# Performance work log

Hardware: AMD Instinct MI355X
Metric: run time of the kernel (lower is better)

## Reference

```python
import jax, jax.numpy as jnp
import numpy as np

N_NODES = 100000
N_EDGES = 3200000
IN_DIM = 128
H1, F1 = 8, 8          # layer1: 8 heads x 8 feats -> concat 64
N_CLASSES = 40         # layer2: 1 head -> classes
NEG_SLOPE = 0.2        # GAT LeakyReLU slope


def setup_inputs() -> dict:
    key = jax.random.key(0)
    ks = jax.random.split(key, 8)
    x = jax.random.normal(ks[0], (N_NODES, IN_DIM), dtype=jnp.float32)
    adj = jax.random.randint(ks[1], (2, N_EDGES), 0, N_NODES, dtype=jnp.int64)
    s1 = 1.0 / np.sqrt(IN_DIM)
    s2 = 1.0 / np.sqrt(H1 * F1)
    W1 = jax.random.normal(ks[2], (IN_DIM, H1 * F1), dtype=jnp.float32) * s1
    a1_src = jax.random.normal(ks[3], (H1, F1), dtype=jnp.float32) * s2
    a1_dst = jax.random.normal(ks[4], (H1, F1), dtype=jnp.float32) * s2
    W2 = jax.random.normal(ks[5], (H1 * F1, N_CLASSES), dtype=jnp.float32) * s2
    a2_src = jax.random.normal(ks[6], (1, N_CLASSES), dtype=jnp.float32) * s2
    a2_dst = jax.random.normal(ks[7], (1, N_CLASSES), dtype=jnp.float32) * s2
    return {"input_matrix": x, "adjacency_coo_matrix": adj,
            "W1": W1, "a1_src": a1_src, "a1_dst": a1_dst,
            "W2": W2, "a2_src": a2_src, "a2_dst": a2_dst}


def gat_layer(x, src, dst, W, a_s, a_d, heads, fdim):
    n = x.shape[0]
    h = (x @ W).reshape(n, heads, fdim)                 # [N,H,F]
    e_src = jnp.sum(h * a_s, axis=-1)                   # [N,H]
    e_dst = jnp.sum(h * a_d, axis=-1)                   # [N,H]
    e = jax.nn.leaky_relu(e_src[src] + e_dst[dst], NEG_SLOPE)  # [E,H]
    m = jax.ops.segment_max(e, dst, num_segments=n)     # per-dst softmax max
    p = jnp.exp(e - m[dst])
    s = jax.ops.segment_sum(p, dst, num_segments=n)
    alpha = p / s[dst]                                  # [E,H]
    out = jax.ops.segment_sum(alpha[:, :, None] * h[src], dst, num_segments=n)
    return out                                          # [N,H,F]


def reference(input_matrix, adjacency_coo_matrix, W1, a1_src, a1_dst, W2, a2_src, a2_dst):
    n = input_matrix.shape[0]
    loops = jnp.arange(n, dtype=adjacency_coo_matrix.dtype)
    src = jnp.concatenate([adjacency_coo_matrix[0], loops])
    dst = jnp.concatenate([adjacency_coo_matrix[1], loops])
    x = gat_layer(input_matrix, src, dst, W1, a1_src, a1_dst, H1, F1)
    x = jax.nn.elu(x.reshape(n, H1 * F1))               # concat heads + ELU
    x = gat_layer(x, src, dst, W2, a2_src, a2_dst, 1, N_CLASSES)
    return jax.nn.log_softmax(x.reshape(n, N_CLASSES), axis=1)
```

## Files before the change

kernel.cpp:

```cpp
#include <hip/hip_runtime.h>
#include <hip/hip_fp16.h>
#include <math.h>

#define NN 100000
#define EE 3200000
#define ET (EE + NN)
#define BKW 128
#define NBK ((NN + BKW - 1) / BKW)
#define BCAP 5120
#define EPB 4096
#define NB_P1 ((EE + EPB - 1) / EPB)
#define NB_G 391
#define NB_A2 ((NN + 23) / 24)

typedef float v2f __attribute__((ext_vector_type(2)));
typedef float v4f __attribute__((ext_vector_type(4)));
typedef _Float16 v8h __attribute__((ext_vector_type(8)));

__device__ __forceinline__ float lrelu(float v) { return fmaxf(v, 0.2f * v); }

__device__ __forceinline__ unsigned char to_fp8(float v) {
  return (unsigned char)(__builtin_amdgcn_cvt_pk_fp8_f32(v, v, 0, false) & 0xff);
}


__global__ __launch_bounds__(256) void k_p1(const int* __restrict__ srcs,
                                            const int* __restrict__ dsts,
                                            int* __restrict__ bcount,
                                            int* __restrict__ bbuf) {
  __shared__ int lcnt[NBK];
  __shared__ int lbase[NBK];
  int tid = threadIdx.x;
  for (int i = tid; i < NBK; i += 256) lcnt[i] = 0;
  __syncthreads();
  int e0 = blockIdx.x * EPB;
  int rank[16], bkt[16], pk[16];
#pragma unroll
  for (int i = 0; i < 16; ++i) {
    int e = e0 + tid + i * 256;
    bkt[i] = -1;
    if (e < EE) {
      int d = dsts[e];
      int s = srcs[e];
      int b = d >> 7;
      rank[i] = atomicAdd(&lcnt[b], 1);
      bkt[i] = b;
      pk[i] = (s << 7) | (d & 127);
    }
  }
  __syncthreads();
  for (int i = tid; i < NBK; i += 256) {
    int c = lcnt[i];
    lbase[i] = c ? atomicAdd(&bcount[i], c) : 0;
  }
  __syncthreads();
#pragma unroll
  for (int i = 0; i < 16; ++i) {
    if (bkt[i] >= 0) {
      bbuf[(size_t)bkt[i] * BCAP + lbase[bkt[i]] + rank[i]] = pk[i];
    }
  }
}

__global__ void k_bscan(const int* __restrict__ bcount, int* __restrict__ bbase) {
  __shared__ int s[1024];
  int t = threadIdx.x;
  int v = 0;
  if (t < NBK) v = bcount[t] + min(BKW, NN - (t << 7));
  s[t] = v;
  __syncthreads();
  for (int off = 1; off < 1024; off <<= 1) {
    int u = (t >= off) ? s[t - off] : 0;
    __syncthreads();
    s[t] += u;
    __syncthreads();
  }
  if (t < NBK) bbase[t] = s[t] - v;
}

__global__ __launch_bounds__(256) void k_p2(const int* __restrict__ bcount,
                                            const int* __restrict__ bbase,
                                            const int* __restrict__ bbuf,
                                            int* __restrict__ offsets,
                                            int* __restrict__ edge_src) {
  __shared__ int cnt[BKW];
  __shared__ int s1[BKW];
  __shared__ int cur[BKW];
  int b = blockIdx.x, tid = threadIdx.x;
  int d0 = b << 7;
  int width = min(BKW, NN - d0);
  int n = bcount[b];
  int base = bbase[b];
  const int* buf = bbuf + (size_t)b * BCAP;
  if (tid < BKW) cnt[tid] = (tid < width) ? 1 : 0;
  __syncthreads();
  for (int i = tid; i < n; i += 256) atomicAdd(&cnt[buf[i] & 127], 1);
  __syncthreads();
  if (tid < BKW) s1[tid] = cnt[tid];
  __syncthreads();
  for (int off = 1; off < BKW; off <<= 1) {
    int u = (tid < BKW && tid >= off) ? s1[tid - off] : 0;
    __syncthreads();
    if (tid < BKW) s1[tid] += u;
    __syncthreads();
  }
  if (tid < width) {
    int excl = s1[tid] - cnt[tid];
    offsets[d0 + tid] = base + excl;
    edge_src[base + excl] = d0 + tid;
    cur[tid] = excl + 1;
  }
  if (b == 0 && tid == 0) offsets[NN] = ET;
  __syncthreads();
  for (int i = tid; i < n; i += 256) {
    int p = buf[i];
    int pos = atomicAdd(&cur[p & 127], 1);
    edge_src[base + pos] = p >> 7;
  }
}


__global__ __launch_bounds__(256) void k_gemm1(
    const float* __restrict__ x, const float* __restrict__ W1,
    const float* __restrict__ a1d,
    unsigned char* __restrict__ P1, float* __restrict__ ed1) {
  __shared__ _Float16 Wb[16 * 64 * 8];
  int tid = threadIdx.x;
  for (int idx = tid; idx < 16 * 64; idx += 256) {
    int f = idx >> 6, l = idx & 63;
    int nt = f >> 2, kk = f & 3;
    int ql = l >> 4, cl = l & 15;
    int col = nt * 16 + cl;
    int k0 = kk * 32 + ql * 8;
    v8h tmp;
#pragma unroll
    for (int j = 0; j < 8; ++j) tmp[j] = (_Float16)W1[(k0 + j) * 64 + col];
    *reinterpret_cast<v8h*>(&Wb[idx * 8]) = tmp;
  }
  __syncthreads();
  int wv = tid >> 6, lane = tid & 63;
  int q = lane >> 4, c = lane & 15;
  v8h bf[16];
#pragma unroll
  for (int f = 0; f < 16; ++f)
    bf[f] = *reinterpret_cast<const v8h*>(&Wb[(f * 64 + lane) * 8]);
  float a1d_l[4];
#pragma unroll
  for (int nt = 0; nt < 4; ++nt) a1d_l[nt] = a1d[nt * 16 + c];
  for (int t = 0; t < 4; ++t) {
    int n0 = blockIdx.x * 256 + wv * 64 + t * 16;
    int row = n0 + c;
    row = (row < NN) ? row : (NN - 1);
    v4f acc[4] = {{0.f,0.f,0.f,0.f},{0.f,0.f,0.f,0.f},{0.f,0.f,0.f,0.f},{0.f,0.f,0.f,0.f}};
#pragma unroll
    for (int kk = 0; kk < 4; ++kk) {
      const float* xp = x + (size_t)row * 128 + kk * 32 + q * 8;
      float4 x0 = *reinterpret_cast<const float4*>(xp);
      float4 x1 = *reinterpret_cast<const float4*>(xp + 4);
      v8h af;
      af[0] = (_Float16)x0.x; af[1] = (_Float16)x0.y;
      af[2] = (_Float16)x0.z; af[3] = (_Float16)x0.w;
      af[4] = (_Float16)x1.x; af[5] = (_Float16)x1.y;
      af[6] = (_Float16)x1.z; af[7] = (_Float16)x1.w;
#pragma unroll
      for (int nt = 0; nt < 4; ++nt)
        acc[nt] = __builtin_amdgcn_mfma_f32_16x16x32_f16(af, bf[nt * 4 + kk], acc[nt], 0, 0, 0);
    }
#pragma unroll
    for (int nt = 0; nt < 4; ++nt) {
#pragma unroll
      for (int r = 0; r < 4; ++r) {
        float val = acc[nt][r];
        float vd = val * a1d_l[nt];
        vd += __shfl_xor(vd, 1); vd += __shfl_xor(vd, 2); vd += __shfl_xor(vd, 4);
        int node = n0 + q * 4 + r;
        if (node < NN) {
          P1[((size_t)node << 6) + nt * 16 + c] = to_fp8(val);
          if ((c & 7) == 0) ed1[node * 8 + 2 * nt + (c >> 3)] = vd;
        }
      }
    }
  }
}


__global__ __launch_bounds__(256) void k_agg1(
    const int* __restrict__ offsets, const int* __restrict__ edge_src,
    const unsigned char* __restrict__ P1, const float* __restrict__ a1s,
    const float* __restrict__ ed1, __half* __restrict__ x2) {
  int wv = threadIdx.x >> 6, lane = threadIdx.x & 63;
  int g = lane >> 3, p = lane & 7;
  int dst = blockIdx.x * 32 + wv * 8 + g;
  float edv = ed1[dst * 8 + p];
  float4 as0 = *reinterpret_cast<const float4*>(a1s + p * 8);
  float4 as1 = *reinterpret_cast<const float4*>(a1s + p * 8 + 4);
  int beg = offsets[dst], end = offsets[dst + 1];
  int deg = end - beg;
  int md = deg;
#pragma unroll
  for (int o = 8; o < 64; o <<= 1) md = max(md, __shfl_xor(md, o, 64));
  float l = 0.f;
  float a[8] = {0.f, 0.f, 0.f, 0.f, 0.f, 0.f, 0.f, 0.f};
  for (int t = 0; t < md; t += 8) {
    int src[8]; uint2 raw[8];
#pragma unroll
    for (int i = 0; i < 8; ++i) {
      int idx = t + i;
      int ci = beg + ((idx < deg) ? idx : (deg - 1));
      src[i] = edge_src[ci];
    }
#pragma unroll
    for (int i = 0; i < 8; ++i)
      raw[i] = *reinterpret_cast<const uint2*>(P1 + ((size_t)src[i] << 6) + (p << 3));
#pragma unroll
    for (int i = 0; i < 8; ++i) {
      v2f f01 = __builtin_amdgcn_cvt_pk_f32_fp8(raw[i].x, false);
      v2f f23 = __builtin_amdgcn_cvt_pk_f32_fp8(raw[i].x, true);
      v2f f45 = __builtin_amdgcn_cvt_pk_f32_fp8(raw[i].y, false);
      v2f f67 = __builtin_amdgcn_cvt_pk_f32_fp8(raw[i].y, true);
      float es = f01.x * as0.x + f01.y * as0.y + f23.x * as0.z + f23.y * as0.w
               + f45.x * as1.x + f45.y * as1.y + f67.x * as1.z + f67.y * as1.w;
      float e = lrelu(es + edv);
      float pr = (t + i < deg) ? __expf(e) : 0.f;
      l += pr;
      a[0] += pr * f01.x; a[1] += pr * f01.y;
      a[2] += pr * f23.x; a[3] += pr * f23.y;
      a[4] += pr * f45.x; a[5] += pr * f45.y;
      a[6] += pr * f67.x; a[7] += pr * f67.y;
    }
  }
  float rl = 1.f / l;
  union { __half h[8]; uint4 u; } pk;
#pragma unroll
  for (int i = 0; i < 8; ++i) {
    float v = a[i] * rl;
    v = (v > 0.f) ? v : (__expf(v) - 1.f);
    pk.h[i] = __float2half(v);
  }
  *reinterpret_cast<uint4*>(x2 + ((size_t)dst << 6) + (p << 3)) = pk.u;
}


__global__ __launch_bounds__(256) void k_gemm2(
    const __half* __restrict__ x2, const float* __restrict__ W2,
    const float* __restrict__ a2s, const float* __restrict__ a2d,
    unsigned char* __restrict__ P2, float* __restrict__ ed2) {
  __shared__ _Float16 Wb[6 * 64 * 8];
  int tid = threadIdx.x;
  for (int idx = tid; idx < 6 * 64; idx += 256) {
    int f = idx >> 6, l = idx & 63;
    int nt = f >> 1, kk = f & 1;
    int ql = l >> 4, cl = l & 15;
    int col = nt * 16 + cl;
    int k0 = kk * 32 + ql * 8;
    v8h tmp;
#pragma unroll
    for (int j = 0; j < 8; ++j)
      tmp[j] = (col < 40) ? (_Float16)W2[(k0 + j) * 40 + col] : (_Float16)0.f;
    *reinterpret_cast<v8h*>(&Wb[idx * 8]) = tmp;
  }
  __syncthreads();
  int wv = tid >> 6, lane = tid & 63;
  int q = lane >> 4, c = lane & 15;
  v8h bf[6];
#pragma unroll
  for (int f = 0; f < 6; ++f)
    bf[f] = *reinterpret_cast<const v8h*>(&Wb[(f * 64 + lane) * 8]);
  float a2s_l[3], a2d_l[3];
#pragma unroll
  for (int nt = 0; nt < 3; ++nt) {
    int n = nt * 16 + c;
    a2s_l[nt] = (n < 40) ? a2s[n] : 0.f;
    a2d_l[nt] = (n < 40) ? a2d[n] : 0.f;
  }
  for (int t = 0; t < 4; ++t) {
    int n0 = blockIdx.x * 256 + wv * 64 + t * 16;
    int row = n0 + c;
    row = (row < NN) ? row : (NN - 1);
    v4f acc[3] = {{0.f,0.f,0.f,0.f},{0.f,0.f,0.f,0.f},{0.f,0.f,0.f,0.f}};
#pragma unroll
    for (int kk = 0; kk < 2; ++kk) {
      v8h af = *reinterpret_cast<const v8h*>(x2 + (size_t)row * 64 + kk * 32 + q * 8);
#pragma unroll
      for (int nt = 0; nt < 3; ++nt)
        acc[nt] = __builtin_amdgcn_mfma_f32_16x16x32_f16(af, bf[nt * 2 + kk], acc[nt], 0, 0, 0);
    }
#pragma unroll
    for (int r = 0; r < 4; ++r) {
      float v0 = acc[0][r], v1 = acc[1][r], v2 = acc[2][r];
      float s = v0 * a2s_l[0] + v1 * a2s_l[1] + v2 * a2s_l[2];
      float d = v0 * a2d_l[0] + v1 * a2d_l[1] + v2 * a2d_l[2];
      s += __shfl_xor(s, 1); s += __shfl_xor(s, 2); s += __shfl_xor(s, 4); s += __shfl_xor(s, 8);
      d += __shfl_xor(d, 1); d += __shfl_xor(d, 2); d += __shfl_xor(d, 4); d += __shfl_xor(d, 8);
      int node = n0 + q * 4 + r;
      if (node < NN) {
        unsigned char* rec = P2 + ((size_t)node << 6);
        if (c < 8) rec[4 + 32 + c] = to_fp8(v2);
        rec[4 + c]      = to_fp8(v0);
        rec[4 + 16 + c] = to_fp8(v1);
        if (c == 0) {
          *reinterpret_cast<__half*>(rec) = __float2half(s);
          ed2[node] = d;
        }
      }
    }
  }
}


__global__ __launch_bounds__(256) void k_agg2(
    const int* __restrict__ offsets, const int* __restrict__ edge_src,
    const unsigned char* __restrict__ P2, const float* __restrict__ ed2,
    float* __restrict__ out) {
  int wv = threadIdx.x >> 6, lane = threadIdx.x & 63;
  int g = lane / 10;
  bool act = g < 6;
  int gg = act ? g : 5;
  int p = lane - g * 10;
  int pp = act ? p : 0;
  int idx = blockIdx.x * 24 + wv * 6 + gg;
  bool live = act && (idx < NN);
  int dst = (idx < NN) ? idx : (NN - 1);
  float edv = ed2[dst];
  int beg = offsets[dst], end = offsets[dst + 1];
  int deg = end - beg;
  int md = deg;
#pragma unroll
  for (int o = 1; o < 64; o <<= 1) md = max(md, __shfl_xor(md, o, 64));
  float l = 0.f;
  float a[4] = {0.f, 0.f, 0.f, 0.f};
  for (int t = 0; t < md; t += 4) {
    int src[4]; unsigned raw[4]; float es[4]; float pr[4];
#pragma unroll
    for (int i = 0; i < 4; ++i) {
      int ix = t + i;
      int ci = beg + ((ix < deg) ? ix : (deg - 1));
      src[i] = edge_src[ci];
    }
#pragma unroll
    for (int i = 0; i < 4; ++i) {
      const unsigned char* rec = P2 + ((size_t)src[i] << 6);
      es[i] = __half2float(*reinterpret_cast<const __half*>(rec));
      raw[i] = *reinterpret_cast<const unsigned*>(rec + 4 + (pp << 2));
    }
#pragma unroll
    for (int i = 0; i < 4; ++i) {
      float e = lrelu(es[i] + edv);
      pr[i] = (t + i < deg) ? __expf(e) : 0.f;
    }
#pragma unroll
    for (int i = 0; i < 4; ++i) {
      v2f f01 = __builtin_amdgcn_cvt_pk_f32_fp8(raw[i], false);
      v2f f23 = __builtin_amdgcn_cvt_pk_f32_fp8(raw[i], true);
      l += pr[i];
      a[0] += pr[i] * f01.x; a[1] += pr[i] * f01.y;
      a[2] += pr[i] * f23.x; a[3] += pr[i] * f23.y;
    }
  }
  float rl = 1.f / l;
  float v0 = a[0] * rl, v1 = a[1] * rl, v2 = a[2] * rl, v3 = a[3] * rl;
  float lmax = fmaxf(fmaxf(v0, v1), fmaxf(v2, v3));
  float red = -INFINITY;
  int base = gg * 10;
#pragma unroll
  for (int j = 0; j < 10; ++j) red = fmaxf(red, __shfl(lmax, base + j, 64));
  float lexp = __expf(v0 - red) + __expf(v1 - red) + __expf(v2 - red) + __expf(v3 - red);
  float se = 0.f;
#pragma unroll
  for (int j = 0; j < 10; ++j) se += __shfl(lexp, base + j, 64);
  float ls = red + __logf(se);
  if (live) {
    float4 o4 = make_float4(v0 - ls, v1 - ls, v2 - ls, v3 - ls);
    *reinterpret_cast<float4*>(out + (size_t)dst * 40 + (p << 2)) = o4;
  }
}


extern "C" void kernel_launch(void* const* d_in, const int* in_sizes, int n_in,
                              void* d_out, int out_size, void* d_ws, size_t ws_size,
                              hipStream_t stream) {
  const float* x   = (const float*)d_in[0];
  const int*   adj = (const int*)d_in[1];
  const float* W1  = (const float*)d_in[2];
  const float* a1s = (const float*)d_in[3];
  const float* a1d = (const float*)d_in[4];
  const float* W2  = (const float*)d_in[5];
  const float* a2s = (const float*)d_in[6];
  const float* a2d = (const float*)d_in[7];
  float* out = (float*)d_out;

  const int* srcs = adj;
  const int* dsts = adj + EE;

  char* w = (char*)d_ws;
  size_t off = 0;
  auto alloc = [&](size_t bytes) -> void* {
    void* p = w + off;
    off = (off + bytes + 255) & ~(size_t)255;
    return p;
  };
  int* offsets      = (int*)alloc((size_t)(NN + 1) * 4);
  int* edge_src     = (int*)alloc((size_t)ET * 4);
  int* bcount       = (int*)alloc((size_t)NBK * 4);
  int* bbase        = (int*)alloc((size_t)NBK * 4);
  unsigned char* P1 = (unsigned char*)alloc((size_t)NN * 64);
  float* ed1        = (float*)alloc((size_t)NN * 8 * 4);
  __half* x2        = (__half*)alloc((size_t)NN * 64 * 2);
  int* bbuf         = (int*)alloc((size_t)NBK * BCAP * 4);
  unsigned char* P2 = P1;
  float* ed2 = ed1;

  hipMemsetAsync(bcount, 0, (size_t)NBK * 4, stream);
  k_p1<<<NB_P1, 256, 0, stream>>>(srcs, dsts, bcount, bbuf);
  k_bscan<<<1, 1024, 0, stream>>>(bcount, bbase);
  k_p2<<<NBK, 256, 0, stream>>>(bcount, bbase, bbuf, offsets, edge_src);

  k_gemm1<<<NB_G, 256, 0, stream>>>(x, W1, a1d, P1, ed1);
  k_agg1<<<NN / 32, 256, 0, stream>>>(offsets, edge_src, P1, a1s, ed1, x2);
  k_gemm2<<<NB_G, 256, 0, stream>>>(x2, W2, a2s, a2d, P2, ed2);
  k_agg2<<<NB_A2, 256, 0, stream>>>(offsets, edge_src, P2, ed2, out);
}
```

Measured before the change: 326.8 us.

## Pack layer-2 records for 8-byte loads and process 12 nodes per wave

The layer-2 fp8 record layout moves the half-precision source score to the end so the class features start at offset 0. This lets each lane load 8 fp8 values with one 8-byte read. The aggregation kernel now gives 5 lanes to each destination node instead of 10, so one wave handles 12 nodes instead of 6 and the block count halves. Fewer lanes are idle (60 of 64 active instead of 60 of 64 but with twice the nodes), and more work shares each wave's edge loop. The cost is that the loop runs to the max degree over 12 nodes, which adds divergence, and each lane now carries more registers.

New measurement: 317.2 us. 1.03x faster.

```diff
diff --git a/kernel.cpp b/kernel.cpp
--- a/kernel.cpp
+++ b/kernel.cpp
@@ -11,7 +11,7 @@
 #define EPB 4096
 #define NB_P1 ((EE + EPB - 1) / EPB)
 #define NB_G 391
-#define NB_A2 ((NN + 23) / 24)
+#define NB_A2 ((NN + 47) / 48)
 
 typedef float v2f __attribute__((ext_vector_type(2)));
 typedef float v4f __attribute__((ext_vector_type(4)));
@@ -295,11 +295,11 @@
       int node = n0 + q * 4 + r;
       if (node < NN) {
         unsigned char* rec = P2 + ((size_t)node << 6);
-        if (c < 8) rec[4 + 32 + c] = to_fp8(v2);
-        rec[4 + c]      = to_fp8(v0);
-        rec[4 + 16 + c] = to_fp8(v1);
+        if (c < 8) rec[32 + c] = to_fp8(v2);
+        rec[c]      = to_fp8(v0);
+        rec[16 + c] = to_fp8(v1);
         if (c == 0) {
-          *reinterpret_cast<__half*>(rec) = __float2half(s);
+          *reinterpret_cast<__half*>(rec + 40) = __float2half(s);
           ed2[node] = d;
         }
       }
@@ -313,12 +313,12 @@
     const unsigned char* __restrict__ P2, const float* __restrict__ ed2,
     float* __restrict__ out) {
   int wv = threadIdx.x >> 6, lane = threadIdx.x & 63;
-  int g = lane / 10;
-  bool act = g < 6;
-  int gg = act ? g : 5;
-  int p = lane - g * 10;
+  int g = lane / 5;
+  bool act = g < 12;
+  int gg = act ? g : 11;
+  int p = lane - g * 5;
   int pp = act ? p : 0;
-  int idx = blockIdx.x * 24 + wv * 6 + gg;
+  int idx = blockIdx.x * 48 + wv * 12 + gg;
   bool live = act && (idx < NN);
   int dst = (idx < NN) ? idx : (NN - 1);
   float edv = ed2[dst];
@@ -328,9 +328,9 @@
 #pragma unroll
   for (int o = 1; o < 64; o <<= 1) md = max(md, __shfl_xor(md, o, 64));
   float l = 0.f;
-  float a[4] = {0.f, 0.f, 0.f, 0.f};
+  float a[8] = {0.f, 0.f, 0.f, 0.f, 0.f, 0.f, 0.f, 0.f};
   for (int t = 0; t < md; t += 4) {
-    int src[4]; unsigned raw[4]; float es[4]; float pr[4];
+    int src[4]; uint2 raw[4]; float es[4]; float pr[4];
 #pragma unroll
     for (int i = 0; i < 4; ++i) {
       int ix = t + i;
@@ -340,8 +340,8 @@
 #pragma unroll
     for (int i = 0; i < 4; ++i) {
       const unsigned char* rec = P2 + ((size_t)src[i] << 6);
-      es[i] = __half2float(*reinterpret_cast<const __half*>(rec));
-      raw[i] = *reinterpret_cast<const unsigned*>(rec + 4 + (pp << 2));
+      es[i] = __half2float(*reinterpret_cast<const __half*>(rec + 40));
+      raw[i] = *reinterpret_cast<const uint2*>(rec + (pp << 3));
     }
 #pragma unroll
     for (int i = 0; i < 4; ++i) {
@@ -350,28 +350,41 @@
     }
 #pragma unroll
     for (int i = 0; i < 4; ++i) {
-      v2f f01 = __builtin_amdgcn_cvt_pk_f32_fp8(raw[i], false);
-      v2f f23 = __builtin_amdgcn_cvt_pk_f32_fp8(raw[i], true);
+      v2f f01 = __builtin_amdgcn_cvt_pk_f32_fp8(raw[i].x, false);
+      v2f f23 = __builtin_amdgcn_cvt_pk_f32_fp8(raw[i].x, true);
+      v2f f45 = __builtin_amdgcn_cvt_pk_f32_fp8(raw[i].y, false);
+      v2f f67 = __builtin_amdgcn_cvt_pk_f32_fp8(raw[i].y, true);
       l += pr[i];
       a[0] += pr[i] * f01.x; a[1] += pr[i] * f01.y;
       a[2] += pr[i] * f23.x; a[3] += pr[i] * f23.y;
+      a[4] += pr[i] * f45.x; a[5] += pr[i] * f45.y;
+      a[6] += pr[i] * f67.x; a[7] += pr[i] * f67.y;
     }
   }
   float rl = 1.f / l;
-  float v0 = a[0] * rl, v1 = a[1] * rl, v2 = a[2] * rl, v3 = a[3] * rl;
-  float lmax = fmaxf(fmaxf(v0, v1), fmaxf(v2, v3));
+  float v[8];
+#pragma unroll
+  for (int i = 0; i < 8; ++i) v[i] = a[i] * rl;
+  float lmax = v[0];
+#pragma unroll
+  for (int i = 1; i < 8; ++i) lmax = fmaxf(lmax, v[i]);
+  int base = gg * 5;
   float red = -INFINITY;
-  int base = gg * 10;
-#pragma unroll
-  for (int j = 0; j < 10; ++j) red = fmaxf(red, __shfl(lmax, base + j, 64));
-  float lexp = __expf(v0 - red) + __expf(v1 - red) + __expf(v2 - red) + __expf(v3 - red);
+#pragma unroll
+  for (int j = 0; j < 5; ++j) red = fmaxf(red, __shfl(lmax, base + j, 64));
+  float lexp = 0.f;
+#pragma unroll
+  for (int i = 0; i < 8; ++i) lexp += __expf(v[i] - red);
   float se = 0.f;
 #pragma unroll
-  for (int j = 0; j < 10; ++j) se += __shfl(lexp, base + j, 64);
+  for (int j = 0; j < 5; ++j) se += __shfl(lexp, base + j, 64);
   float ls = red + __logf(se);
   if (live) {
-    float4 o4 = make_float4(v0 - ls, v1 - ls, v2 - ls, v3 - ls);
-    *reinterpret_cast<float4*>(out + (size_t)dst * 40 + (p << 2)) = o4;
+    float4 o0 = make_float4(v[0] - ls, v[1] - ls, v[2] - ls, v[3] - ls);
+    float4 o1 = make_float4(v[4] - ls, v[5] - ls, v[6] - ls, v[7] - ls);
+    float* op = out + (size_t)dst * 40 + (p << 3);
+    *reinterpret_cast<float4*>(op)     = o0;
+    *reinterpret_cast<float4*>(op + 4) = o1;
   }
 }
 
```
